# Kernel optimization log

Hardware: AMD Instinct MI355X
Metric: run time of the kernel (lower is better)

## Reference

```python
import jax, jax.numpy as jnp
import numpy as np

NUM_HEADS = 16
BLOCK_SIZE = 64
NUM_GLOBAL_TOKENS = 64
WINDOW_SIZE = 256
NUM_RANDOM_BLOCKS = 3
BATCH = 2
SEQ_LEN = 4096
EMBED_DIM = 1024


def _alibi_slopes(n):
    # power-of-2 head count path of _compute_alibi_slopes
    base = 2.0 ** (-(2.0 ** (-(np.log2(n) - 3.0))))
    return jnp.asarray([base ** i for i in range(1, n + 1)], dtype=jnp.float32)


def _build_block_indices():
    nb = SEQ_LEN // BLOCK_SIZE
    ngb = NUM_GLOBAL_TOKENS // BLOCK_SIZE
    wb = WINDOW_SIZE // BLOCK_SIZE
    mb = 2 * wb + 1 + NUM_RANDOM_BLOCKS
    rng = np.random.default_rng(0)
    out = np.full((nb, mb), -1, dtype=np.int64)
    for qb in range(nb):
        attended = set(range(ngb))  # global blocks handled separately
        idx = 0
        for kb in range(max(ngb, qb - wb), min(nb, qb + wb + 1)):
            if kb not in attended:
                out[qb, idx] = kb
                attended.add(kb)
                idx += 1
        cand = [b for b in range(ngb, nb) if b not in attended]
        pick = rng.choice(len(cand), size=min(NUM_RANDOM_BLOCKS, len(cand)), replace=False)
        for j in pick:
            out[qb, idx] = cand[j]
            idx += 1
    return jnp.asarray(out)


def setup_inputs() -> dict:
    key = jax.random.key(0)
    ks = jax.random.split(key, 5)
    s = 0.02
    x = jax.random.normal(ks[0], (BATCH, SEQ_LEN, EMBED_DIM), jnp.float32)
    Wq = jax.random.normal(ks[1], (EMBED_DIM, EMBED_DIM), jnp.float32) * s
    Wk = jax.random.normal(ks[2], (EMBED_DIM, EMBED_DIM), jnp.float32) * s
    Wv = jax.random.normal(ks[3], (EMBED_DIM, EMBED_DIM), jnp.float32) * s
    Wo = jax.random.normal(ks[4], (EMBED_DIM, EMBED_DIM), jnp.float32) * s
    return {"x": x, "Wq": Wq, "Wk": Wk, "Wv": Wv, "Wo": Wo,
            "block_indices": _build_block_indices()}


def reference(x, Wq, Wk, Wv, Wo, block_indices):
    B, S, E = x.shape
    H = NUM_HEADS
    Dh = E // H
    G = NUM_GLOBAL_TOKENS
    BS = BLOCK_SIZE
    scale = 1.0 / np.sqrt(Dh)

    def split_heads(t):
        return t.reshape(B, S, H, Dh).transpose(0, 2, 1, 3)  # [B,H,S,Dh]

    q = split_heads(x @ Wq)
    k = split_heads(x @ Wk)
    v = split_heads(x @ Wv)

    slopes = _alibi_slopes(H)  # [H]
    pos = jnp.arange(S, dtype=jnp.float32)

    # ---- global tokens: full attention over all keys ----
    sg = jnp.einsum('bhgd,bhsd->bhgs', q[:, :, :G], k) * scale
    bias_g = -slopes[:, None, None] * jnp.abs(pos[:G, None] - pos[None, :])  # [H,G,S]
    pg = jax.nn.softmax(sg + bias_g[None], axis=-1)
    out_g = jnp.einsum('bhgs,bhsd->bhgd', pg, v)  # [B,H,G,Dh]

    # ---- sparse queries: global KV + gathered sparse blocks ----
    nb = S // BS
    ngb = G // BS
    nqb = nb - ngb
    bi = block_indices[ngb:]           # [nqb, MB], -1 = padding
    mb = bi.shape[1]
    bsafe = jnp.maximum(bi, 0)

    kb = k.reshape(B, H, nb, BS, Dh)
    vb = v.reshape(B, H, nb, BS, Dh)
    kg = kb[:, :, bsafe].reshape(B, H, nqb, mb * BS, Dh)
    vg = vb[:, :, bsafe].reshape(B, H, nqb, mb * BS, Dh)
    kglob = jnp.broadcast_to(k[:, :, None, :G], (B, H, nqb, G, Dh))
    vglob = jnp.broadcast_to(v[:, :, None, :G], (B, H, nqb, G, Dh))
    kcat = jnp.concatenate([kglob, kg], axis=3)  # [B,H,nqb,G+mb*BS,Dh]
    vcat = jnp.concatenate([vglob, vg], axis=3)

    qn = q[:, :, G:].reshape(B, H, nqb, BS, Dh)
    scores = jnp.einsum('bhqmd,bhqnd->bhqmn', qn, kcat) * scale

    qpos = (G + jnp.arange(nqb * BS, dtype=jnp.float32)).reshape(nqb, BS)
    loc_pos = (bsafe[:, :, None] * BS + jnp.arange(BS)[None, None, :]).reshape(nqb, mb * BS).astype(jnp.float32)
    kpos = jnp.concatenate([jnp.broadcast_to(pos[:G][None], (nqb, G)), loc_pos], axis=1)
    bias = -slopes[:, None, None, None] * jnp.abs(qpos[None, :, :, None] - kpos[None, :, None, :])  # [H,nqb,BS,Kt]

    valid = jnp.concatenate([jnp.ones((nqb, G), bool), jnp.repeat(bi >= 0, BS, axis=1)], axis=1)
    scores = jnp.where(valid[None, None, :, None, :], scores + bias[None], -jnp.inf)
    p = jax.nn.softmax(scores, axis=-1)
    out_s = jnp.einsum('bhqmn,bhqnd->bhqmd', p, vcat).reshape(B, H, S - G, Dh)

    out = jnp.concatenate([out_g, out_s], axis=2)  # [B,H,S,Dh]
    out = out.transpose(0, 2, 1, 3).reshape(B, S, E)
    return out @ Wo
```

## Files before the change

### kernel.cpp

```cpp
#include <hip/hip_runtime.h>
#include <stdint.h>

typedef __attribute__((ext_vector_type(8))) short short8;
typedef __attribute__((ext_vector_type(4))) float f32x4;
typedef __attribute__((ext_vector_type(8))) unsigned short u16x8;
typedef __attribute__((ext_vector_type(2))) unsigned int u32x2;

#define DEV static __device__ __forceinline__

DEV unsigned short f2bf(float f) {
  union { float f; uint32_t u; } v; v.f = f;
  uint32_t r = v.u + 0x7FFFu + ((v.u >> 16) & 1u);
  return (unsigned short)(r >> 16);
}

DEV void gload16(const void* g, void* l) {
  __builtin_amdgcn_global_load_lds(
      (const __attribute__((address_space(1))) void*)g,
      (__attribute__((address_space(3))) void*)l, 16, 0, 0);
}

__global__ __launch_bounds__(256) void prep_kernel(const float* __restrict__ x,
                                                   unsigned short* __restrict__ xb,
                                                   const float* __restrict__ Wq,
                                                   const float* __restrict__ Wk,
                                                   const float* __restrict__ Wv,
                                                   const float* __restrict__ Wo,
                                                   unsigned short* __restrict__ wt) {
  __shared__ float tile[64][65];
  int t = threadIdx.x;
  if (blockIdx.x < 4096) {
    int i = blockIdx.x * 256 + t;
    f32x4 a = ((const f32x4*)x)[2 * i];
    f32x4 b = ((const f32x4*)x)[2 * i + 1];
    u16x8 o;
    o[0] = f2bf(a[0]); o[1] = f2bf(a[1]); o[2] = f2bf(a[2]); o[3] = f2bf(a[3]);
    o[4] = f2bf(b[0]); o[5] = f2bf(b[1]); o[6] = f2bf(b[2]); o[7] = f2bf(b[3]);
    ((u16x8*)xb)[i] = o;
    return;
  }
  int flat = blockIdx.x - 4096;
  int bn = flat & 15, bk = (flat >> 4) & 15, z = flat >> 8;
  const float* W = (z == 0) ? Wq : (z == 1) ? Wk : (z == 2) ? Wv : Wo;
  unsigned short* dst = wt + (size_t)z * 1024 * 1024;
  int c = t & 63, rr = t >> 6;
#pragma unroll
  for (int p = 0; p < 16; ++p) {
    int r = p * 4 + rr;
    tile[r][c] = W[(size_t)(bk * 64 + r) * 1024 + bn * 64 + c];
  }
  __syncthreads();
#pragma unroll
  for (int p = 0; p < 16; ++p) {
    int r2 = p * 4 + rr;
    dst[(size_t)(bn * 64 + r2) * 1024 + bk * 64 + c] = f2bf(tile[c][r2]);
  }
}

__global__ __launch_bounds__(256, 2) void gemm_qkv(const unsigned short* __restrict__ A,
                                                   const unsigned short* __restrict__ wt,
                                                   unsigned short* __restrict__ Qb,
                                                   unsigned short* __restrict__ Kb,
                                                   unsigned short* __restrict__ Vtb,
                                                   float qscale) {
  constexpr int K = 1024;
  __shared__ __align__(16) unsigned short As[2][128 * 64];
  __shared__ __align__(16) unsigned short Bs[2][128 * 64];
  int flat = blockIdx.x + 24 * blockIdx.y;
  int xcd = flat & 7, idx = flat >> 3;
  int bm = xcd * 8 + (idx & 7);
  int bn = idx >> 3;
  int which = bn >> 3, bnn = bn & 7;
  int tid = threadIdx.x, lane = tid & 63, w = tid >> 6;
  int wr = w >> 1, wc = w & 1;
  f32x4 acc[4][4] = {};

  int sr[4], soff[4];
#pragma unroll
  for (int i = 0; i < 4; ++i) {
    int ci = w * 4 + i;
    int r = ci * 8 + (lane >> 3);
    sr[i] = r;
    soff[i] = ((lane & 7) ^ (r & 7)) * 8;
  }
  const unsigned short* Arow = A + (size_t)(bm * 128) * K;
  const unsigned short* Brow = wt + (size_t)which * 1048576 + (size_t)(bnn * 128) * K;

  auto STAGE = [&](int bi, int k0) {
#pragma unroll
    for (int i = 0; i < 4; ++i) {
      gload16(Arow + (size_t)sr[i] * K + k0 + soff[i], &As[bi][(w * 4 + i) * 512]);
      gload16(Brow + (size_t)sr[i] * K + k0 + soff[i], &Bs[bi][(w * 4 + i) * 512]);
    }
  };

  STAGE(0, 0);
  for (int kt = 0; kt < 16; ++kt) {
    int cur = kt & 1;
    asm volatile("s_waitcnt vmcnt(0)" ::: "memory");
    __builtin_amdgcn_s_barrier();
    __builtin_amdgcn_sched_barrier(0);
    if (kt < 15) STAGE(cur ^ 1, (kt + 1) * 64);
    __builtin_amdgcn_sched_barrier(0);
    short8 af[2][4], bfr[2][4];
#pragma unroll
    for (int c = 0; c < 2; ++c) {
#pragma unroll
      for (int m = 0; m < 4; ++m) {
        int cc = (lane >> 4) + 4 * c;
        int ra = wr * 64 + m * 16 + (lane & 15);
        af[c][m] = *(const short8*)(&As[cur][ra * 64 + ((cc ^ (ra & 7)) * 8)]);
        int rb = wc * 64 + m * 16 + (lane & 15);
        bfr[c][m] = *(const short8*)(&Bs[cur][rb * 64 + ((cc ^ (rb & 7)) * 8)]);
      }
    }
#pragma unroll
    for (int c = 0; c < 2; ++c)
#pragma unroll
      for (int m = 0; m < 4; ++m)
#pragma unroll
        for (int n = 0; n < 4; ++n)
          acc[m][n] = __builtin_amdgcn_mfma_f32_16x16x32_bf16(af[c][m], bfr[c][n], acc[m][n], 0, 0, 0);
  }

  int rbase = bm * 128 + wr * 64;
  int cbase = bnn * 128 + wc * 64;
#pragma unroll
  for (int m = 0; m < 4; ++m)
#pragma unroll
    for (int n = 0; n < 4; ++n) {
      int row0 = rbase + m * 16 + (lane >> 4) * 4;
      int col = cbase + n * 16 + (lane & 15);
      int h = col >> 6, d = col & 63;
      int b = row0 >> 12, s0 = row0 & 4095;
      if (which == 0) {
#pragma unroll
        for (int reg = 0; reg < 4; ++reg)
          Qb[((size_t)(b * 16 + h) * 4096 + s0 + reg) * 64 + d] = f2bf(acc[m][n][reg] * qscale);
      } else if (which == 1) {
#pragma unroll
        for (int reg = 0; reg < 4; ++reg)
          Kb[((size_t)(b * 16 + h) * 4096 + s0 + reg) * 64 + d] = f2bf(acc[m][n][reg]);
      } else {
        u32x2 pk;
        asm("v_cvt_pk_bf16_f32 %0, %1, %2" : "=v"(pk[0]) : "v"(acc[m][n][0]), "v"(acc[m][n][1]));
        asm("v_cvt_pk_bf16_f32 %0, %1, %2" : "=v"(pk[1]) : "v"(acc[m][n][2]), "v"(acc[m][n][3]));
        *(u32x2*)(Vtb + ((((size_t)(b * 16 + h) * 64 + (s0 >> 6)) * 64 + d) * 64 + (s0 & 63))) = pk;
      }
    }
}

__global__ __launch_bounds__(256, 2) void gemm_out(const unsigned short* __restrict__ A,
                                                   const unsigned short* __restrict__ Bt,
                                                   float* __restrict__ dst) {
  constexpr int K = 1024;
  __shared__ __align__(16) unsigned short As[2][128 * 64];
  __shared__ __align__(16) unsigned short Bs[2][128 * 64];
  int flat = blockIdx.x + 8 * blockIdx.y;
  int xcd = flat & 7, idx = flat >> 3;
  int bm = xcd * 8 + (idx & 7);
  int bn = idx >> 3;
  int tid = threadIdx.x, lane = tid & 63, w = tid >> 6;
  int wr = w >> 1, wc = w & 1;
  f32x4 acc[4][4] = {};

  int sr[4], soff[4];
#pragma unroll
  for (int i = 0; i < 4; ++i) {
    int ci = w * 4 + i;
    int r = ci * 8 + (lane >> 3);
    sr[i] = r;
    soff[i] = ((lane & 7) ^ (r & 7)) * 8;
  }
  const unsigned short* Arow = A + (size_t)(bm * 128) * K;
  const unsigned short* Brow = Bt + (size_t)(bn * 128) * K;

  auto STAGE = [&](int bi, int k0) {
#pragma unroll
    for (int i = 0; i < 4; ++i) {
      gload16(Arow + (size_t)sr[i] * K + k0 + soff[i], &As[bi][(w * 4 + i) * 512]);
      gload16(Brow + (size_t)sr[i] * K + k0 + soff[i], &Bs[bi][(w * 4 + i) * 512]);
    }
  };

  STAGE(0, 0);
  for (int kt = 0; kt < 16; ++kt) {
    int cur = kt & 1;
    asm volatile("s_waitcnt vmcnt(0)" ::: "memory");
    __builtin_amdgcn_s_barrier();
    __builtin_amdgcn_sched_barrier(0);
    if (kt < 15) STAGE(cur ^ 1, (kt + 1) * 64);
    __builtin_amdgcn_sched_barrier(0);
    short8 af[2][4], bfr[2][4];
#pragma unroll
    for (int c = 0; c < 2; ++c) {
#pragma unroll
      for (int m = 0; m < 4; ++m) {
        int cc = (lane >> 4) + 4 * c;
        int ra = wr * 64 + m * 16 + (lane & 15);
        af[c][m] = *(const short8*)(&As[cur][ra * 64 + ((cc ^ (ra & 7)) * 8)]);
        int rb = wc * 64 + m * 16 + (lane & 15);
        bfr[c][m] = *(const short8*)(&Bs[cur][rb * 64 + ((cc ^ (rb & 7)) * 8)]);
      }
    }
#pragma unroll
    for (int c = 0; c < 2; ++c)
#pragma unroll
      for (int m = 0; m < 4; ++m)
#pragma unroll
        for (int n = 0; n < 4; ++n)
          acc[m][n] = __builtin_amdgcn_mfma_f32_16x16x32_bf16(af[c][m], bfr[c][n], acc[m][n], 0, 0, 0);
  }

  int rbase = bm * 128 + wr * 64;
  int cbase = bn * 128 + wc * 64;
#pragma unroll
  for (int m = 0; m < 4; ++m)
#pragma unroll
    for (int n = 0; n < 4; ++n) {
      int row0 = rbase + m * 16 + (lane >> 4) * 4;
      int col = cbase + n * 16 + (lane & 15);
#pragma unroll
      for (int reg = 0; reg < 4; ++reg)
        dst[(size_t)(row0 + reg) * 1024 + col] = acc[m][n][reg];
    }
}

__global__ __launch_bounds__(256) void attn_kernel(const unsigned short* __restrict__ Qh,
                            const unsigned short* __restrict__ Kh,
                            const unsigned short* __restrict__ Vbt,
                            const int* __restrict__ bidx,
                            unsigned short* __restrict__ attn_out,
                            float* __restrict__ Opart,
                            float* __restrict__ lpart) {
  __shared__ __align__(16) unsigned short Ks[3][64 * 64];
  __shared__ __align__(16) unsigned short Vs[2][64 * 64];
  int flat = blockIdx.x + 71 * blockIdx.y;
  int nf = (flat & 7) * 284 + (flat >> 3);
  int gx = nf % 71, bh = nf / 71;
  int h = bh & 15;
  int tid = threadIdx.x, lane = tid & 63, w = tid >> 6;
  int q = lane & 15, g = lane >> 4;
  float slope2 = exp2f(-0.5f * (float)(h + 1)) * 1.44269504f;

  int qb, nkb;
  int vlist;
  if (gx < 63) {
    qb = gx + 1;
    int v = -1;
    if (lane == 0) v = 0;
    else if (lane <= 12) v = bidx[qb * 12 + (lane - 1)];
    vlist = v;
    unsigned long long msk = __ballot(v >= 0);
    nkb = __builtin_popcountll(msk & 0x1FFFull);
  } else {
    qb = 0;
    nkb = 8;
    vlist = (gx - 63) * 8 + lane;
  }

  int qrow = qb * 64 + w * 16 + q;
  const unsigned short* qptr = Qh + ((size_t)bh * 4096 + qrow) * 64 + g * 8;
  short8 qf0 = *(const short8*)qptr;
  short8 qf1 = *(const short8*)(qptr + 32);

  float qposf = (float)qrow;
  float sq = slope2 * qposf;
  float er[4][4];
#pragma unroll
  for (int ct = 0; ct < 4; ++ct)
#pragma unroll
    for (int r = 0; r < 4; ++r) er[ct][r] = slope2 * (float)(ct * 16 + r);

  float psum = 0.f;
  f32x4 accO[4] = {};

  const unsigned short* Kbh = Kh + (size_t)bh * 4096 * 64;
  const unsigned short* Vbh = Vbt + (size_t)bh * 4096 * 64;

  int srr[2], so[2];
#pragma unroll
  for (int i = 0; i < 2; ++i) {
    int ci = w * 2 + i;
    int r = ci * 8 + (lane >> 3);
    srr[i] = r;
    so[i] = ((lane & 7) ^ (r & 7)) * 8;
  }
  auto STAGE_K = [&](int bi, int kb) {
    const unsigned short* kbase = Kbh + (size_t)kb * 4096;
#pragma unroll
    for (int i = 0; i < 2; ++i)
      gload16(kbase + srr[i] * 64 + so[i], &Ks[bi][(w * 2 + i) * 512]);
  };
  auto STAGE_V = [&](int bi, int kb) {
    const unsigned short* vbase = Vbh + (size_t)kb * 4096;
#pragma unroll
    for (int i = 0; i < 2; ++i)
      gload16(vbase + srr[i] * 64 + so[i], &Vs[bi][(w * 2 + i) * 512]);
  };

  STAGE_K(0, __builtin_amdgcn_readlane(vlist, 0));
  STAGE_V(0, __builtin_amdgcn_readlane(vlist, 0));
  STAGE_K(1, __builtin_amdgcn_readlane(vlist, 1));

  for (int it = 0; it < nkb; ++it) {
    int curK = it % 3, curV = it & 1;
    int kb = __builtin_amdgcn_readlane(vlist, it);
    if (it + 1 < nkb) {
      asm volatile("s_waitcnt vmcnt(2)" ::: "memory");
    } else {
      asm volatile("s_waitcnt vmcnt(0)" ::: "memory");
    }
    __builtin_amdgcn_s_barrier();
    __builtin_amdgcn_sched_barrier(0);
    if (it + 1 < nkb) STAGE_V((it + 1) & 1, __builtin_amdgcn_readlane(vlist, it + 1));
    if (it + 2 < nkb) STAGE_K((it + 2) % 3, __builtin_amdgcn_readlane(vlist, it + 2));

    float kb4g = (float)(kb * 64 + 4 * g);
    float d_[4][4];
    if (kb != qb) {
      if (kb < qb) {
        float t = __builtin_fmaf(slope2, kb4g, -sq);
#pragma unroll
        for (int ct = 0; ct < 4; ++ct)
#pragma unroll
          for (int r = 0; r < 4; ++r) d_[ct][r] = t + er[ct][r];
      } else {
        float t = sq - slope2 * kb4g;
#pragma unroll
        for (int ct = 0; ct < 4; ++ct)
#pragma unroll
          for (int r = 0; r < 4; ++r) d_[ct][r] = t - er[ct][r];
      }
    } else {
      float db = qposf - kb4g;
#pragma unroll
      for (int ct = 0; ct < 4; ++ct)
#pragma unroll
        for (int r = 0; r < 4; ++r)
          d_[ct][r] = -slope2 * fabsf(db - (float)(ct * 16 + r));
    }

    float pv[4][4];
    __builtin_amdgcn_s_setprio(1);
#pragma unroll
    for (int ct = 0; ct < 4; ++ct) {
      int kr = ct * 16 + q;
      short8 kf0 = *(const short8*)(&Ks[curK][kr * 64 + ((g ^ (kr & 7)) * 8)]);
      short8 kf1 = *(const short8*)(&Ks[curK][kr * 64 + (((g + 4) ^ (kr & 7)) * 8)]);
      f32x4 cin = {d_[ct][0], d_[ct][1], d_[ct][2], d_[ct][3]};
      f32x4 s = __builtin_amdgcn_mfma_f32_16x16x32_bf16(kf0, qf0, cin, 0, 0, 0);
      s = __builtin_amdgcn_mfma_f32_16x16x32_bf16(kf1, qf1, s, 0, 0, 0);
#pragma unroll
      for (int r = 0; r < 4; ++r) {
        float p = exp2f(s[r]);
        pv[ct][r] = p;
        psum += p;
      }
    }
    __builtin_amdgcn_s_setprio(0);

    uint32_t pkw[4][2];
#pragma unroll
    for (int ct = 0; ct < 4; ++ct) {
      asm("v_cvt_pk_bf16_f32 %0, %1, %2" : "=v"(pkw[ct][0]) : "v"(pv[ct][0]), "v"(pv[ct][1]));
      asm("v_cvt_pk_bf16_f32 %0, %1, %2" : "=v"(pkw[ct][1]) : "v"(pv[ct][2]), "v"(pv[ct][3]));
    }
    bool odd = (tid & 16) != 0;
    short8 pa[2];
#pragma unroll
    for (int f = 0; f < 2; ++f) {
      uint32_t s0 = pkw[2 * f][0], s1 = pkw[2 * f][1];
      uint32_t t0 = pkw[2 * f + 1][0], t1 = pkw[2 * f + 1][1];
      asm("v_permlane32_swap_b32 %0, %1" : "+v"(s0), "+v"(t0));
      asm("v_permlane32_swap_b32 %0, %1" : "+v"(s1), "+v"(t1));
      uint32_t xs0 = (uint32_t)__shfl_xor((int)s0, 16, 64);
      uint32_t xs1 = (uint32_t)__shfl_xor((int)s1, 16, 64);
      uint32_t xt0 = (uint32_t)__shfl_xor((int)t0, 16, 64);
      uint32_t xt1 = (uint32_t)__shfl_xor((int)t1, 16, 64);
      union { uint32_t w[4]; short8 v; } u;
      u.w[0] = odd ? xt0 : s0;
      u.w[1] = odd ? xt1 : s1;
      u.w[2] = odd ? t0 : xs0;
      u.w[3] = odd ? t1 : xs1;
      pa[f] = u.v;
    }

    __builtin_amdgcn_s_setprio(1);
#pragma unroll
    for (int dt = 0; dt < 4; ++dt) {
      int dr = dt * 16 + q;
      short8 vf0 = *(const short8*)(&Vs[curV][dr * 64 + ((g ^ (dr & 7)) * 8)]);
      short8 vf1 = *(const short8*)(&Vs[curV][dr * 64 + (((g + 4) ^ (dr & 7)) * 8)]);
      accO[dt] = __builtin_amdgcn_mfma_f32_16x16x32_bf16(pa[0], vf0, accO[dt], 0, 0, 0);
      accO[dt] = __builtin_amdgcn_mfma_f32_16x16x32_bf16(pa[1], vf1, accO[dt], 0, 0, 0);
    }
    __builtin_amdgcn_s_setprio(0);
  }

  float lt = psum;
  lt += __shfl_xor(lt, 16, 64);
  lt += __shfl_xor(lt, 32, 64);

  int b = bh >> 4;
  if (gx < 63) {
#pragma unroll
    for (int reg = 0; reg < 4; ++reg) {
      float ls = __shfl(lt, 4 * g + reg, 64);
      float rl = 1.0f / ls;
      int row = qb * 64 + w * 16 + 4 * g + reg;
#pragma unroll
      for (int dt = 0; dt < 4; ++dt) {
        int col = h * 64 + dt * 16 + q;
        attn_out[((size_t)b * 4096 + row) * 1024 + col] = f2bf(accO[dt][reg] * rl);
      }
    }
  } else {
    int chunk = gx - 63;
    float* Op = Opart + (size_t)(bh * 8 + chunk) * 64 * 64;
    float* lp = lpart + (size_t)(bh * 8 + chunk) * 64;
#pragma unroll
    for (int reg = 0; reg < 4; ++reg) {
      int row = w * 16 + 4 * g + reg;
#pragma unroll
      for (int dt = 0; dt < 4; ++dt) {
        int col = dt * 16 + q;
        Op[row * 64 + col] = accO[dt][reg];
      }
    }
    if (g == 0) lp[w * 16 + q] = lt;
  }
}

__global__ void merge_qb0(const float* __restrict__ Opart, const float* __restrict__ lpart,
                          unsigned short* __restrict__ attn_out) {
  int bh = blockIdx.x;
  int tid = threadIdx.x;
  int row = tid >> 2, cg = tid & 3;
  const float* lp = lpart + (size_t)bh * 8 * 64;
  float L = 0.f;
#pragma unroll
  for (int c = 0; c < 8; ++c) L += lp[c * 64 + row];
  float rL = 1.0f / L;
  int b = bh >> 4, h = bh & 15;
  f32x4 acc0 = {}, acc1 = {}, acc2 = {}, acc3 = {};
#pragma unroll
  for (int c = 0; c < 8; ++c) {
    const float* Op = Opart + ((size_t)(bh * 8 + c) * 64 + row) * 64 + cg * 16;
    acc0 += ((const f32x4*)Op)[0];
    acc1 += ((const f32x4*)Op)[1];
    acc2 += ((const f32x4*)Op)[2];
    acc3 += ((const f32x4*)Op)[3];
  }
  unsigned short* out = attn_out + ((size_t)b * 4096 + row) * 1024 + h * 64 + cg * 16;
#pragma unroll
  for (int j = 0; j < 4; ++j) {
    out[j] = f2bf(acc0[j] * rL);
    out[4 + j] = f2bf(acc1[j] * rL);
    out[8 + j] = f2bf(acc2[j] * rL);
    out[12 + j] = f2bf(acc3[j] * rL);
  }
}

extern "C" void kernel_launch(void* const* d_in, const int* in_sizes, int n_in,
                              void* d_out, int out_size, void* d_ws, size_t ws_size,
                              hipStream_t stream) {
  const float* x = (const float*)d_in[0];
  const float* Wq = (const float*)d_in[1];
  const float* Wk = (const float*)d_in[2];
  const float* Wv = (const float*)d_in[3];
  const float* Wo = (const float*)d_in[4];
  const int* bidx = (const int*)d_in[5];

  char* ws = (char*)d_ws;
  unsigned short* xb = (unsigned short*)(ws);
  unsigned short* wt = (unsigned short*)(ws + 16777216);
  unsigned short* Qb = (unsigned short*)(ws + 25165824);
  unsigned short* Kb = (unsigned short*)(ws + 41943040);
  unsigned short* Vtb = (unsigned short*)(ws + 58720256);
  unsigned short* attnb = (unsigned short*)(ws + 75497472);
  float* Opart = (float*)(ws);
  float* lpart = (float*)(ws + 4194304);

  prep_kernel<<<5120, 256, 0, stream>>>(x, xb, Wq, Wk, Wv, Wo, wt);
  gemm_qkv<<<dim3(24, 64), 256, 0, stream>>>(xb, wt, Qb, Kb, Vtb, 0.18033688f);
  attn_kernel<<<dim3(71, 32), 256, 0, stream>>>(Qb, Kb, Vtb, bidx, attnb, Opart, lpart);
  merge_qb0<<<32, 256, 0, stream>>>(Opart, lpart, attnb);
  gemm_out<<<dim3(8, 64), 256, 0, stream>>>(attnb, wt + 3145728, (float*)d_out);
}
```

Before: 165.5 us.

## Use 256x256 8-wave QKV GEMM tiles with phased pipelining and reorder out-GEMM prefetch

```diff
diff --git a/kernel.cpp b/kernel.cpp
--- a/kernel.cpp
+++ b/kernel.cpp
@@ -57,80 +57,105 @@
   }
 }
 
-__global__ __launch_bounds__(256, 2) void gemm_qkv(const unsigned short* __restrict__ A,
-                                                   const unsigned short* __restrict__ wt,
-                                                   unsigned short* __restrict__ Qb,
-                                                   unsigned short* __restrict__ Kb,
-                                                   unsigned short* __restrict__ Vtb,
-                                                   float qscale) {
+__global__ __launch_bounds__(512, 1) void gemm_qkv8(const unsigned short* __restrict__ A,
+                                                    const unsigned short* __restrict__ wt,
+                                                    unsigned short* __restrict__ Qb,
+                                                    unsigned short* __restrict__ Kb,
+                                                    unsigned short* __restrict__ Vtb,
+                                                    float qscale) {
   constexpr int K = 1024;
-  __shared__ __align__(16) unsigned short As[2][128 * 64];
-  __shared__ __align__(16) unsigned short Bs[2][128 * 64];
-  int flat = blockIdx.x + 24 * blockIdx.y;
+  extern __shared__ unsigned short lds[];
+  int flat = blockIdx.x;
   int xcd = flat & 7, idx = flat >> 3;
-  int bm = xcd * 8 + (idx & 7);
-  int bn = idx >> 3;
-  int which = bn >> 3, bnn = bn & 7;
+  int bm = xcd * 4 + (idx & 3);
+  int bn = idx >> 2;
+  int which = bn >> 2, bnl = bn & 3;
   int tid = threadIdx.x, lane = tid & 63, w = tid >> 6;
-  int wr = w >> 1, wc = w & 1;
-  f32x4 acc[4][4] = {};
-
-  int sr[4], soff[4];
-#pragma unroll
-  for (int i = 0; i < 4; ++i) {
-    int ci = w * 4 + i;
-    int r = ci * 8 + (lane >> 3);
-    sr[i] = r;
-    soff[i] = ((lane & 7) ^ (r & 7)) * 8;
-  }
-  const unsigned short* Arow = A + (size_t)(bm * 128) * K;
-  const unsigned short* Brow = wt + (size_t)which * 1048576 + (size_t)(bnn * 128) * K;
-
-  auto STAGE = [&](int bi, int k0) {
-#pragma unroll
-    for (int i = 0; i < 4; ++i) {
-      gload16(Arow + (size_t)sr[i] * K + k0 + soff[i], &As[bi][(w * 4 + i) * 512]);
-      gload16(Brow + (size_t)sr[i] * K + k0 + soff[i], &Bs[bi][(w * 4 + i) * 512]);
+  int wm = w >> 2, wn = w & 3;
+  int q = lane & 15, g = lane >> 4;
+  f32x4 acc[8][4] = {};
+
+  const unsigned short* Arow = A + (size_t)(bm * 256) * K;
+  const unsigned short* Brow = wt + (size_t)which * 1048576 + (size_t)(bnl * 256) * K;
+
+  auto STG = [&](unsigned short* dstTile, const unsigned short* src, int h, int k0) {
+#pragma unroll
+    for (int i = 0; i < 2; ++i) {
+      int ci = w * 2 + i;
+      int r = h * 128 + ci * 8 + (lane >> 3);
+      gload16(src + (size_t)r * K + k0 + (((lane & 7) ^ (r & 7)) * 8),
+              dstTile + h * 8192 + ci * 512);
     }
   };
 
-  STAGE(0, 0);
-  for (int kt = 0; kt < 16; ++kt) {
-    int cur = kt & 1;
-    asm volatile("s_waitcnt vmcnt(0)" ::: "memory");
-    __builtin_amdgcn_s_barrier();
-    __builtin_amdgcn_sched_barrier(0);
-    if (kt < 15) STAGE(cur ^ 1, (kt + 1) * 64);
-    __builtin_amdgcn_sched_barrier(0);
-    short8 af[2][4], bfr[2][4];
-#pragma unroll
-    for (int c = 0; c < 2; ++c) {
-#pragma unroll
-      for (int m = 0; m < 4; ++m) {
-        int cc = (lane >> 4) + 4 * c;
-        int ra = wr * 64 + m * 16 + (lane & 15);
-        af[c][m] = *(const short8*)(&As[cur][ra * 64 + ((cc ^ (ra & 7)) * 8)]);
-        int rb = wc * 64 + m * 16 + (lane & 15);
-        bfr[c][m] = *(const short8*)(&Bs[cur][rb * 64 + ((cc ^ (rb & 7)) * 8)]);
-      }
-    }
-#pragma unroll
-    for (int c = 0; c < 2; ++c)
-#pragma unroll
-      for (int m = 0; m < 4; ++m)
-#pragma unroll
-        for (int n = 0; n < 4; ++n)
-          acc[m][n] = __builtin_amdgcn_mfma_f32_16x16x32_bf16(af[c][m], bfr[c][n], acc[m][n], 0, 0, 0);
-  }
-
-  int rbase = bm * 128 + wr * 64;
-  int cbase = bnn * 128 + wc * 64;
-#pragma unroll
-  for (int m = 0; m < 4; ++m)
+  unsigned short* Ab0 = lds;
+  unsigned short* Ab1 = lds + 16384;
+  unsigned short* Bb0 = lds + 32768;
+  unsigned short* Bb1 = lds + 49152;
+
+  STG(Ab0, Arow, 0, 0);  STG(Ab0, Arow, 1, 0);
+  STG(Bb0, Brow, 0, 0);  STG(Bb0, Brow, 1, 0);
+  STG(Ab1, Arow, 0, 64); STG(Ab1, Arow, 1, 64);
+  STG(Bb1, Brow, 0, 64); STG(Bb1, Brow, 1, 64);
+  asm volatile("s_waitcnt vmcnt(8)" ::: "memory");
+  __builtin_amdgcn_s_barrier();
+
+  short8 bfr[4][2];
+  for (int t = 0; t < 16; ++t) {
+    unsigned short* Ac = (t & 1) ? Ab1 : Ab0;
+    unsigned short* Ao = (t & 1) ? Ab0 : Ab1;
+    unsigned short* Bc = (t & 1) ? Bb1 : Bb0;
+
+#define QPHASE(qd)                                                                       \
+    {                                                                                    \
+      short8 af[2][2];                                                                   \
+      _Pragma("unroll") for (int mi = 0; mi < 2; ++mi)                                   \
+        _Pragma("unroll") for (int kk = 0; kk < 2; ++kk) {                               \
+          int lr = wm * 128 + (2 * (qd) + mi) * 16 + q;                                  \
+          af[mi][kk] = *(const short8*)(&Ac[lr * 64 + (((kk * 4 + g) ^ (lr & 7)) * 8)]); \
+        }                                                                                \
+      if ((qd) == 0) {                                                                   \
+        _Pragma("unroll") for (int n = 0; n < 4; ++n)                                    \
+          _Pragma("unroll") for (int kk = 0; kk < 2; ++kk) {                             \
+            int lrb = wn * 64 + n * 16 + q;                                              \
+            bfr[n][kk] = *(const short8*)(&Bc[lrb * 64 + (((kk * 4 + g) ^ (lrb & 7)) * 8)]); \
+          }                                                                              \
+      }                                                                                  \
+      if ((qd) == 0 && t >= 1 && t + 1 < 16) STG(Ao, Arow, 0, (t + 1) * 64);             \
+      if ((qd) == 1 && t >= 1 && t + 1 < 16) STG(Ao, Arow, 1, (t + 1) * 64);             \
+      if ((qd) == 2 && t + 2 < 16) STG(Bc, Brow, 0, (t + 2) * 64);                       \
+      if ((qd) == 3 && t + 2 < 16) STG(Bc, Brow, 1, (t + 2) * 64);                       \
+      if ((qd) == 3) {                                                                   \
+        if (t >= 14) { asm volatile("s_waitcnt vmcnt(0)" ::: "memory"); }                \
+        else         { asm volatile("s_waitcnt vmcnt(4)" ::: "memory"); }                \
+      }                                                                                  \
+      __builtin_amdgcn_s_barrier();                                                      \
+      asm volatile("s_waitcnt lgkmcnt(0)" ::: "memory");                                 \
+      __builtin_amdgcn_sched_barrier(0);                                                 \
+      __builtin_amdgcn_s_setprio(1);                                                     \
+      _Pragma("unroll") for (int mi = 0; mi < 2; ++mi)                                   \
+        _Pragma("unroll") for (int n = 0; n < 4; ++n)                                    \
+          _Pragma("unroll") for (int kk = 0; kk < 2; ++kk)                               \
+            acc[2 * (qd) + mi][n] = __builtin_amdgcn_mfma_f32_16x16x32_bf16(             \
+                af[mi][kk], bfr[n][kk], acc[2 * (qd) + mi][n], 0, 0, 0);                 \
+      __builtin_amdgcn_s_setprio(0);                                                     \
+      __builtin_amdgcn_s_barrier();                                                      \
+    }
+    QPHASE(0)
+    QPHASE(1)
+    QPHASE(2)
+    QPHASE(3)
+#undef QPHASE
+  }
+
+  int rbase = bm * 256 + wm * 128;
+  int cb = bnl * 256 + wn * 64;
+#pragma unroll
+  for (int m = 0; m < 8; ++m)
 #pragma unroll
     for (int n = 0; n < 4; ++n) {
-      int row0 = rbase + m * 16 + (lane >> 4) * 4;
-      int col = cbase + n * 16 + (lane & 15);
+      int row0 = rbase + m * 16 + g * 4;
+      int col = cb + n * 16 + q;
       int h = col >> 6, d = col & 63;
       int b = row0 >> 12, s0 = row0 & 4095;
       if (which == 0) {
@@ -186,10 +211,13 @@
   STAGE(0, 0);
   for (int kt = 0; kt < 16; ++kt) {
     int cur = kt & 1;
-    asm volatile("s_waitcnt vmcnt(0)" ::: "memory");
+    if (kt < 15) {
+      STAGE(cur ^ 1, (kt + 1) * 64);
+      asm volatile("s_waitcnt vmcnt(8)" ::: "memory");
+    } else {
+      asm volatile("s_waitcnt vmcnt(0)" ::: "memory");
+    }
     __builtin_amdgcn_s_barrier();
-    __builtin_amdgcn_sched_barrier(0);
-    if (kt < 15) STAGE(cur ^ 1, (kt + 1) * 64);
     __builtin_amdgcn_sched_barrier(0);
     short8 af[2][4], bfr[2][4];
 #pragma unroll
@@ -210,6 +238,8 @@
 #pragma unroll
         for (int n = 0; n < 4; ++n)
           acc[m][n] = __builtin_amdgcn_mfma_f32_16x16x32_bf16(af[c][m], bfr[c][n], acc[m][n], 0, 0, 0);
+    __builtin_amdgcn_s_barrier();
+    __builtin_amdgcn_sched_barrier(0);
   }
 
   int rbase = bm * 128 + wr * 64;
@@ -482,8 +512,11 @@
   float* Opart = (float*)(ws);
   float* lpart = (float*)(ws + 4194304);
 
+  hipFuncSetAttribute((const void*)gemm_qkv8,
+                      hipFuncAttributeMaxDynamicSharedMemorySize, 131072);
+
   prep_kernel<<<5120, 256, 0, stream>>>(x, xb, Wq, Wk, Wv, Wo, wt);
-  gemm_qkv<<<dim3(24, 64), 256, 0, stream>>>(xb, wt, Qb, Kb, Vtb, 0.18033688f);
+  gemm_qkv8<<<384, 512, 131072, stream>>>(xb, wt, Qb, Kb, Vtb, 0.18033688f);
   attn_kernel<<<dim3(71, 32), 256, 0, stream>>>(Qb, Kb, Vtb, bidx, attnb, Opart, lpart);
   merge_qb0<<<32, 256, 0, stream>>>(Opart, lpart, attnb);
   gemm_out<<<dim3(8, 64), 256, 0, stream>>>(attnb, wt + 3145728, (float*)d_out);
```

Result: slower. 175.6 us (+6.1%).
